# Kernel tuning notes

Hardware: AMD Instinct MI355X
Metric: run time of the kernel (lower is better)

The kernel has to match this reference:

```python
import jax, jax.numpy as jnp
import numpy as np

B, T, D, H, E, K = 4, 1024, 1024, 2048, 8, 2  # batch, tokens, model_dim, ffn hidden, experts, top-k


def setup_inputs() -> dict:
    key = jax.random.key(0)
    k0, k1, k2, k3 = jax.random.split(key, 4)
    return {
        "x": jax.random.normal(k0, (B, T, D), dtype=jnp.float32),
        "wg": jax.random.normal(k1, (D, E), dtype=jnp.float32) * 0.02,   # gate projection
        "w1": jax.random.normal(k2, (E, D, H), dtype=jnp.float32) * 0.02,  # expert fc1
        "b1": jnp.zeros((E, H), dtype=jnp.float32),
        "w2": jax.random.normal(k3, (E, H, D), dtype=jnp.float32) * 0.02,  # expert fc2
        "b2": jnp.zeros((E, D), dtype=jnp.float32),
    }


def _moe(x, wg, w1, b1, w2, b2):
    N = B * T
    xt = x.reshape(N, D)
    # --- gating: softmax scores, top-2 selection, normalize selected gates ---
    logits = xt @ wg                         # [N, E]
    scores = jax.nn.softmax(logits, axis=-1)
    vals, idx = jax.lax.top_k(scores, K)     # [N, K]
    vals = vals / jnp.sum(vals, axis=-1, keepdims=True)
    # combine weights: [N, E], nonzero only at the top-k experts per token
    combine = jnp.zeros((N, E), dtype=xt.dtype).at[
        jnp.arange(N)[:, None], idx
    ].add(vals)
    # --- expert FFN (activation_fn is identity per source) ---
    h = jnp.einsum('nd,edh->neh', xt, w1) + b1   # [N, E, H]
    o = jnp.einsum('neh,ehd->ned', h, w2) + b2   # [N, E, D]
    # --- combine / scatter back ---
    y = jnp.einsum('ne,ned->nd', combine, o)     # [N, D]
    return y.reshape(B, T, D)


def reference(x, wg, w1, b1, w2, b2):
    y = _moe(x, wg, w1, b1, w2, b2)              # [B, T, D]
    s = jnp.sum(y, axis=2)                       # [B, T]
    return jax.nn.log_softmax(s, axis=1)
```

## Files before the change

### kernel.cpp

```cpp
#include <hip/hip_runtime.h>
#include <stdint.h>

#define B_ 4
#define T_ 1024
#define D_ 1024
#define H_ 2048
#define E_ 8

__device__ __forceinline__ void stage16(const float* g, float* l) {
    __builtin_amdgcn_global_load_lds(
        (const __attribute__((address_space(1))) uint32_t*)g,
        (__attribute__((address_space(3))) uint32_t*)l, 16, 0, 0);
}

__global__ __launch_bounds__(256) void w2sum_kernel(const float* __restrict__ w2,
                                                    float* __restrict__ w2sum) {
    __shared__ float buf[3][4 * D_];
    const int wid = threadIdx.x >> 6, lane = threadIdx.x & 63;
    const float* src = w2 + ((size_t)blockIdx.x * 32 + wid) * D_ + lane * 4;

#define A_STAGE(k)                                                        \
    {                                                                     \
        const float* s_ = src + (size_t)(k) * 4 * D_;                     \
        float* d_ = &buf[(k) % 3][wid * D_];                              \
        stage16(s_,       d_);       stage16(s_ + 256, d_ + 256);         \
        stage16(s_ + 512, d_ + 512); stage16(s_ + 768, d_ + 768);         \
    }

    A_STAGE(0); A_STAGE(1);
    float accs[8];
#pragma unroll
    for (int k = 0; k < 8; ++k) {
        if (k < 7) asm volatile("s_waitcnt vmcnt(4)" ::: "memory");
        else       asm volatile("s_waitcnt vmcnt(0)" ::: "memory");
        if (k < 6) A_STAGE(k + 2);
        const float* row = &buf[k % 3][wid * D_];
        float acc = 0.f;
#pragma unroll
        for (int j = 0; j < 4; ++j) {
            float4 a = *(const float4*)&row[j * 256 + lane * 4];
            acc += a.x + a.y + a.z + a.w;
        }
#pragma unroll
        for (int off = 32; off >= 1; off >>= 1) acc += __shfl_xor(acc, off, 64);
        accs[k] = acc;
    }
#undef A_STAGE
    if (lane == 0) {
        const int r0 = blockIdx.x * 32 + wid;
#pragma unroll
        for (int k = 0; k < 8; ++k) w2sum[r0 + k * 4] = accs[k];
    }
}

__global__ __launch_bounds__(256) void v_build_kernel(const float* __restrict__ w1,
                                                      const float* __restrict__ w2sum,
                                                      const float* __restrict__ b1,
                                                      const float* __restrict__ b2,
                                                      float* __restrict__ vT,
                                                      float* __restrict__ c) {
    __shared__ float buf[2][4 * H_];
    const int bid = blockIdx.x;
    const int e   = bid >> 6;
    const int d0  = (bid & 63) * 16;
    const int wid = threadIdx.x >> 6, lane = threadIdx.x & 63;
    const float* src = w1 + ((size_t)e * D_ + d0 + wid) * H_ + lane * 4;

    const float4* wsp = (const float4*)(w2sum + (size_t)e * H_) + lane;
    float4 s0 = wsp[0],   s1 = wsp[64],  s2 = wsp[128], s3 = wsp[192],
           s4 = wsp[256], s5 = wsp[320], s6 = wsp[384], s7 = wsp[448];
    asm volatile("" ::: "memory");

#define B_STAGE(k)                                                         \
    {                                                                      \
        const float* s_ = src + (size_t)(k) * 4 * H_;                      \
        float* d_ = &buf[(k) & 1][wid * H_];                               \
        stage16(s_,        d_);        stage16(s_ + 256,  d_ + 256);       \
        stage16(s_ + 512,  d_ + 512);  stage16(s_ + 768,  d_ + 768);       \
        stage16(s_ + 1024, d_ + 1024); stage16(s_ + 1280, d_ + 1280);      \
        stage16(s_ + 1536, d_ + 1536); stage16(s_ + 1792, d_ + 1792);      \
    }

    B_STAGE(0); B_STAGE(1);
    float accs[4];
#pragma unroll
    for (int k = 0; k < 4; ++k) {
        if (k < 3) asm volatile("s_waitcnt vmcnt(8)" ::: "memory");
        else       asm volatile("s_waitcnt vmcnt(0)" ::: "memory");
        const float* row = &buf[k & 1][wid * H_];
        float acc;
        {
            float4 a0 = *(const float4*)&row[0 * 256 + lane * 4];
            float4 a1 = *(const float4*)&row[1 * 256 + lane * 4];
            float4 a2 = *(const float4*)&row[2 * 256 + lane * 4];
            float4 a3 = *(const float4*)&row[3 * 256 + lane * 4];
            float4 a4 = *(const float4*)&row[4 * 256 + lane * 4];
            float4 a5 = *(const float4*)&row[5 * 256 + lane * 4];
            float4 a6 = *(const float4*)&row[6 * 256 + lane * 4];
            float4 a7 = *(const float4*)&row[7 * 256 + lane * 4];
            acc = a0.x*s0.x + a0.y*s0.y + a0.z*s0.z + a0.w*s0.w
                + a1.x*s1.x + a1.y*s1.y + a1.z*s1.z + a1.w*s1.w
                + a2.x*s2.x + a2.y*s2.y + a2.z*s2.z + a2.w*s2.w
                + a3.x*s3.x + a3.y*s3.y + a3.z*s3.z + a3.w*s3.w
                + a4.x*s4.x + a4.y*s4.y + a4.z*s4.z + a4.w*s4.w
                + a5.x*s5.x + a5.y*s5.y + a5.z*s5.z + a5.w*s5.w
                + a6.x*s6.x + a6.y*s6.y + a6.z*s6.z + a6.w*s6.w
                + a7.x*s7.x + a7.y*s7.y + a7.z*s7.z + a7.w*s7.w;
        }
#pragma unroll
        for (int off = 32; off >= 1; off >>= 1) acc += __shfl_xor(acc, off, 64);
        accs[k] = acc;
        if (k < 2) B_STAGE(k + 2);
    }
#undef B_STAGE
    if (lane == 0) {
#pragma unroll
        for (int k = 0; k < 4; ++k)
            vT[(size_t)(d0 + k * 4 + wid) * E_ + e] = accs[k];
    }

    if ((bid & 63) == 0 && wid == 0) {
        const float4* bp = (const float4*)(b1 + (size_t)e * H_) + lane;
        float4 q0 = bp[0],   q1 = bp[64],  q2 = bp[128], q3 = bp[192],
               q4 = bp[256], q5 = bp[320], q6 = bp[384], q7 = bp[448];
        float s = q0.x*s0.x + q0.y*s0.y + q0.z*s0.z + q0.w*s0.w
                + q1.x*s1.x + q1.y*s1.y + q1.z*s1.z + q1.w*s1.w
                + q2.x*s2.x + q2.y*s2.y + q2.z*s2.z + q2.w*s2.w
                + q3.x*s3.x + q3.y*s3.y + q3.z*s3.z + q3.w*s3.w
                + q4.x*s4.x + q4.y*s4.y + q4.z*s4.z + q4.w*s4.w
                + q5.x*s5.x + q5.y*s5.y + q5.z*s5.z + q5.w*s5.w
                + q6.x*s6.x + q6.y*s6.y + q6.z*s6.z + q6.w*s6.w
                + q7.x*s7.x + q7.y*s7.y + q7.z*s7.z + q7.w*s7.w;
        const float4* cp = (const float4*)(b2 + (size_t)e * D_) + lane;
#pragma unroll
        for (int j = 0; j < 4; ++j) {
            float4 bb = cp[j * 64];
            s += bb.x + bb.y + bb.z + bb.w;
        }
#pragma unroll
        for (int off = 32; off >= 1; off >>= 1) s += __shfl_xor(s, off, 64);
        if (lane == 0) c[e] = s;
    }
}

__global__ __launch_bounds__(256) void token_kernel(
    const float* __restrict__ x,  const float* __restrict__ wg,
    const float* __restrict__ vT, const float* __restrict__ cbuf,
    float* __restrict__ sbuf)
{
    __shared__ float wgl[D_ * E_];
    __shared__ float vtl[D_ * E_];
    const int wid = threadIdx.x >> 6, lane = threadIdx.x & 63;

#pragma unroll
    for (int r = 0; r < 8; ++r) {
        int base = r * 1024 + wid * 256;
        stage16(wg + base + lane * 4, wgl + base);
        stage16(vT + base + lane * 4, vtl + base);
    }
    asm volatile("s_waitcnt vmcnt(0)" ::: "memory");
    __syncthreads();

    const int half = lane & 1;
    const int rrow = lane >> 1;

#pragma unroll
    for (int t = 0; t < 4; ++t) {
        const int n = blockIdx.x * 16 + wid * 4 + t;
        const float* xg = x + (size_t)n * D_ + rrow;
        float ag0 = 0.f, ag1 = 0.f, ag2 = 0.f, ag3 = 0.f;
        float av0 = 0.f, av1 = 0.f, av2 = 0.f, av3 = 0.f;
#pragma unroll
        for (int k = 0; k < 32; ++k) {
            float xs = xg[32 * k];
            const int o = (32 * k + rrow) * 8 + half * 4;
            float4 w4 = *(const float4*)&wgl[o];
            float4 v4 = *(const float4*)&vtl[o];
            ag0 += xs * w4.x; ag1 += xs * w4.y; ag2 += xs * w4.z; ag3 += xs * w4.w;
            av0 += xs * v4.x; av1 += xs * v4.y; av2 += xs * v4.z; av3 += xs * v4.w;
        }
#pragma unroll
        for (int off = 2; off <= 32; off <<= 1) {
            ag0 += __shfl_xor(ag0, off, 64); ag1 += __shfl_xor(ag1, off, 64);
            ag2 += __shfl_xor(ag2, off, 64); ag3 += __shfl_xor(ag3, off, 64);
            av0 += __shfl_xor(av0, off, 64); av1 += __shfl_xor(av1, off, 64);
            av2 += __shfl_xor(av2, off, 64); av3 += __shfl_xor(av3, off, 64);
        }
        float g4 = __shfl(ag0, 1, 64), g5 = __shfl(ag1, 1, 64),
              g6 = __shfl(ag2, 1, 64), g7 = __shfl(ag3, 1, 64);
        float h4 = __shfl(av0, 1, 64), h5 = __shfl(av1, 1, 64),
              h6 = __shfl(av2, 1, 64), h7 = __shfl(av3, 1, 64);
        if (lane == 0) {
            float lg[E_] = {ag0, ag1, ag2, ag3, g4, g5, g6, g7};
            float dv[E_] = {av0, av1, av2, av3, h4, h5, h6, h7};
            float m0 = lg[0]; int i0 = 0;
#pragma unroll
            for (int q = 1; q < E_; ++q) if (lg[q] > m0) { m0 = lg[q]; i0 = q; }
            float m1 = -3.0e38f; int i1 = 0;
#pragma unroll
            for (int q = 0; q < E_; ++q) if (q != i0 && lg[q] > m1) { m1 = lg[q]; i1 = q; }
            float dv0 = 0.f, dv1 = 0.f, c0v = 0.f, c1v = 0.f;
#pragma unroll
            for (int q = 0; q < E_; ++q) {
                if (q == i0) { dv0 += dv[q]; c0v += cbuf[q]; }
                if (q == i1) { dv1 += dv[q]; c1v += cbuf[q]; }
            }
            float g1w = 1.f / (1.f + expf(m0 - m1));
            sbuf[n] = (1.f - g1w) * (dv0 + c0v) + g1w * (dv1 + c1v);
        }
    }
}

__global__ __launch_bounds__(256) void lsm_kernel(const float* __restrict__ s,
                                                  float* __restrict__ out) {
    int brow = threadIdx.x >> 6;
    int lane = threadIdx.x & 63;
    const float* row = s + (size_t)brow * T_;
    float vals[16];
    float mx = -3.0e38f;
#pragma unroll
    for (int k = 0; k < 16; ++k) {
        vals[k] = row[lane + 64 * k];
        mx = fmaxf(mx, vals[k]);
    }
#pragma unroll
    for (int off = 32; off >= 1; off >>= 1) mx = fmaxf(mx, __shfl_xor(mx, off, 64));
    float sm = 0.f;
#pragma unroll
    for (int k = 0; k < 16; ++k) sm += expf(vals[k] - mx);
#pragma unroll
    for (int off = 32; off >= 1; off >>= 1) sm += __shfl_xor(sm, off, 64);
    float lse = mx + logf(sm);
#pragma unroll
    for (int k = 0; k < 16; ++k) out[(size_t)brow * T_ + lane + 64 * k] = vals[k] - lse;
}

extern "C" void kernel_launch(void* const* d_in, const int* in_sizes, int n_in,
                              void* d_out, int out_size, void* d_ws, size_t ws_size,
                              hipStream_t stream) {
    const float* x  = (const float*)d_in[0];
    const float* wg = (const float*)d_in[1];
    const float* w1 = (const float*)d_in[2];
    const float* b1 = (const float*)d_in[3];
    const float* w2 = (const float*)d_in[4];
    const float* b2 = (const float*)d_in[5];
    float* out = (float*)d_out;

    float* ws     = (float*)d_ws;
    float* w2sum  = ws;
    float* vT     = ws + 16384;
    float* cbuf   = ws + 24576;
    float* sbuf   = ws + 24592;

    w2sum_kernel<<<dim3(512), dim3(256), 0, stream>>>(w2, w2sum);
    v_build_kernel<<<dim3(512), dim3(256), 0, stream>>>(w1, w2sum, b1, b2, vT, cbuf);
    token_kernel<<<dim3(256), dim3(256), 0, stream>>>(x, wg, vT, cbuf, sbuf);
    lsm_kernel<<<dim3(1), dim3(256), 0, stream>>>(sbuf, out);
}
```

Baseline: 41.61 us.

## Fuse w2 row-sum and w1 projection into one kernel with atomic accumulation

Merges the w2 row-sum and the w1·w2sum projection into a single kernel. Each block owns a 32-wide slice of H for one expert, reduces the matching w2 rows into shared memory, then streams the w1 columns for that slice and accumulates partial vT and bias terms with atomicAdd. This drops one kernel launch and the global round trip of w2sum, at the cost of a memset and roughly a million atomic adds whose float ordering is nondeterministic. The token kernel also changes to process two tokens per wave over twice as many blocks, reusing the shared-memory weight loads across both tokens.

```diff
diff --git a/kernel.cpp b/kernel.cpp
--- a/kernel.cpp
+++ b/kernel.cpp
@@ -13,133 +13,104 @@
         (__attribute__((address_space(3))) uint32_t*)l, 16, 0, 0);
 }
 
-__global__ __launch_bounds__(256) void w2sum_kernel(const float* __restrict__ w2,
-                                                    float* __restrict__ w2sum) {
-    __shared__ float buf[3][4 * D_];
-    const int wid = threadIdx.x >> 6, lane = threadIdx.x & 63;
-    const float* src = w2 + ((size_t)blockIdx.x * 32 + wid) * D_ + lane * 4;
-
-#define A_STAGE(k)                                                        \
-    {                                                                     \
-        const float* s_ = src + (size_t)(k) * 4 * D_;                     \
-        float* d_ = &buf[(k) % 3][wid * D_];                              \
-        stage16(s_,       d_);       stage16(s_ + 256, d_ + 256);         \
-        stage16(s_ + 512, d_ + 512); stage16(s_ + 768, d_ + 768);         \
-    }
-
-    A_STAGE(0); A_STAGE(1);
-    float accs[8];
-#pragma unroll
-    for (int k = 0; k < 8; ++k) {
-        if (k < 7) asm volatile("s_waitcnt vmcnt(4)" ::: "memory");
-        else       asm volatile("s_waitcnt vmcnt(0)" ::: "memory");
-        if (k < 6) A_STAGE(k + 2);
-        const float* row = &buf[k % 3][wid * D_];
-        float acc = 0.f;
-#pragma unroll
-        for (int j = 0; j < 4; ++j) {
-            float4 a = *(const float4*)&row[j * 256 + lane * 4];
-            acc += a.x + a.y + a.z + a.w;
-        }
-#pragma unroll
-        for (int off = 32; off >= 1; off >>= 1) acc += __shfl_xor(acc, off, 64);
-        accs[k] = acc;
-    }
-#undef A_STAGE
-    if (lane == 0) {
-        const int r0 = blockIdx.x * 32 + wid;
-#pragma unroll
-        for (int k = 0; k < 8; ++k) w2sum[r0 + k * 4] = accs[k];
-    }
-}
-
-__global__ __launch_bounds__(256) void v_build_kernel(const float* __restrict__ w1,
-                                                      const float* __restrict__ w2sum,
-                                                      const float* __restrict__ b1,
-                                                      const float* __restrict__ b2,
-                                                      float* __restrict__ vT,
-                                                      float* __restrict__ c) {
-    __shared__ float buf[2][4 * H_];
+__global__ __launch_bounds__(256) void ab_kernel(
+    const float* __restrict__ w1, const float* __restrict__ b1,
+    const float* __restrict__ w2, const float* __restrict__ b2,
+    float* __restrict__ vT, float* __restrict__ cbuf)
+{
+    __shared__ float buf[3][4096];
+    __shared__ float wssum[32];
     const int bid = blockIdx.x;
     const int e   = bid >> 6;
-    const int d0  = (bid & 63) * 16;
+    const int j0  = (bid & 63) * 32;
     const int wid = threadIdx.x >> 6, lane = threadIdx.x & 63;
-    const float* src = w1 + ((size_t)e * D_ + d0 + wid) * H_ + lane * 4;
-
-    const float4* wsp = (const float4*)(w2sum + (size_t)e * H_) + lane;
-    float4 s0 = wsp[0],   s1 = wsp[64],  s2 = wsp[128], s3 = wsp[192],
-           s4 = wsp[256], s5 = wsp[320], s6 = wsp[384], s7 = wsp[448];
-    asm volatile("" ::: "memory");
-
-#define B_STAGE(k)                                                         \
-    {                                                                      \
-        const float* s_ = src + (size_t)(k) * 4 * H_;                      \
-        float* d_ = &buf[(k) & 1][wid * H_];                               \
-        stage16(s_,        d_);        stage16(s_ + 256,  d_ + 256);       \
-        stage16(s_ + 512,  d_ + 512);  stage16(s_ + 768,  d_ + 768);       \
-        stage16(s_ + 1024, d_ + 1024); stage16(s_ + 1280, d_ + 1280);      \
-        stage16(s_ + 1536, d_ + 1536); stage16(s_ + 1792, d_ + 1792);      \
-    }
-
-    B_STAGE(0); B_STAGE(1);
-    float accs[4];
-#pragma unroll
-    for (int k = 0; k < 4; ++k) {
-        if (k < 3) asm volatile("s_waitcnt vmcnt(8)" ::: "memory");
+
+    {
+        const float* src = w2 + ((size_t)(e * H_ + j0) + wid) * D_ + lane * 4;
+#define P1_STAGE(k) { const float* s_ = src + (size_t)(k) * 4 * D_;           \
+                      float* d_ = &buf[(k) % 3][wid * 1024];                  \
+                      stage16(s_, d_);         stage16(s_ + 256, d_ + 256);   \
+                      stage16(s_ + 512, d_ + 512); stage16(s_ + 768, d_ + 768); }
+        P1_STAGE(0); P1_STAGE(1);
+        float accs[8];
+#pragma unroll
+        for (int k = 0; k < 8; ++k) {
+            if (k < 7) asm volatile("s_waitcnt vmcnt(4)" ::: "memory");
+            else       asm volatile("s_waitcnt vmcnt(0)" ::: "memory");
+            if (k < 6) P1_STAGE(k + 2);
+            const float* row = &buf[k % 3][wid * 1024];
+            float acc = 0.f;
+#pragma unroll
+            for (int j = 0; j < 4; ++j) {
+                float4 a = *(const float4*)&row[j * 256 + lane * 4];
+                acc += a.x + a.y + a.z + a.w;
+            }
+#pragma unroll
+            for (int off = 32; off >= 1; off >>= 1) acc += __shfl_xor(acc, off, 64);
+            accs[k] = acc;
+        }
+#undef P1_STAGE
+        if (lane == 0) {
+#pragma unroll
+            for (int k = 0; k < 8; ++k) wssum[wid + k * 4] = accs[k];
+        }
+    }
+    __syncthreads();
+
+    const float4 wsv = *(const float4*)&wssum[(lane & 7) * 4];
+    const float* w1base = w1 + (size_t)e * D_ * H_ + j0 + (lane & 7) * 4;
+
+#define P2_STAGE(t) {                                                          \
+        const int rb_ = wid * 256 + (t) * 32;                                  \
+        float* d_ = &buf[(t) % 3][wid * 1024];                                 \
+        const float* s_ = w1base + (size_t)(rb_ + (lane >> 3)) * H_;           \
+        stage16(s_,               d_);                                         \
+        stage16(s_ + (size_t) 8 * H_, d_ + 256);                               \
+        stage16(s_ + (size_t)16 * H_, d_ + 512);                               \
+        stage16(s_ + (size_t)24 * H_, d_ + 768); }
+
+    P2_STAGE(0); P2_STAGE(1);
+    float p[8][4];
+#pragma unroll
+    for (int t = 0; t < 8; ++t) {
+        if (t < 7) asm volatile("s_waitcnt vmcnt(4)" ::: "memory");
         else       asm volatile("s_waitcnt vmcnt(0)" ::: "memory");
-        const float* row = &buf[k & 1][wid * H_];
-        float acc;
-        {
-            float4 a0 = *(const float4*)&row[0 * 256 + lane * 4];
-            float4 a1 = *(const float4*)&row[1 * 256 + lane * 4];
-            float4 a2 = *(const float4*)&row[2 * 256 + lane * 4];
-            float4 a3 = *(const float4*)&row[3 * 256 + lane * 4];
-            float4 a4 = *(const float4*)&row[4 * 256 + lane * 4];
-            float4 a5 = *(const float4*)&row[5 * 256 + lane * 4];
-            float4 a6 = *(const float4*)&row[6 * 256 + lane * 4];
-            float4 a7 = *(const float4*)&row[7 * 256 + lane * 4];
-            acc = a0.x*s0.x + a0.y*s0.y + a0.z*s0.z + a0.w*s0.w
-                + a1.x*s1.x + a1.y*s1.y + a1.z*s1.z + a1.w*s1.w
-                + a2.x*s2.x + a2.y*s2.y + a2.z*s2.z + a2.w*s2.w
-                + a3.x*s3.x + a3.y*s3.y + a3.z*s3.z + a3.w*s3.w
-                + a4.x*s4.x + a4.y*s4.y + a4.z*s4.z + a4.w*s4.w
-                + a5.x*s5.x + a5.y*s5.y + a5.z*s5.z + a5.w*s5.w
-                + a6.x*s6.x + a6.y*s6.y + a6.z*s6.z + a6.w*s6.w
-                + a7.x*s7.x + a7.y*s7.y + a7.z*s7.z + a7.w*s7.w;
-        }
-#pragma unroll
-        for (int off = 32; off >= 1; off >>= 1) acc += __shfl_xor(acc, off, 64);
-        accs[k] = acc;
-        if (k < 2) B_STAGE(k + 2);
-    }
-#undef B_STAGE
-    if (lane == 0) {
-#pragma unroll
-        for (int k = 0; k < 4; ++k)
-            vT[(size_t)(d0 + k * 4 + wid) * E_ + e] = accs[k];
-    }
-
-    if ((bid & 63) == 0 && wid == 0) {
-        const float4* bp = (const float4*)(b1 + (size_t)e * H_) + lane;
-        float4 q0 = bp[0],   q1 = bp[64],  q2 = bp[128], q3 = bp[192],
-               q4 = bp[256], q5 = bp[320], q6 = bp[384], q7 = bp[448];
-        float s = q0.x*s0.x + q0.y*s0.y + q0.z*s0.z + q0.w*s0.w
-                + q1.x*s1.x + q1.y*s1.y + q1.z*s1.z + q1.w*s1.w
-                + q2.x*s2.x + q2.y*s2.y + q2.z*s2.z + q2.w*s2.w
-                + q3.x*s3.x + q3.y*s3.y + q3.z*s3.z + q3.w*s3.w
-                + q4.x*s4.x + q4.y*s4.y + q4.z*s4.z + q4.w*s4.w
-                + q5.x*s5.x + q5.y*s5.y + q5.z*s5.z + q5.w*s5.w
-                + q6.x*s6.x + q6.y*s6.y + q6.z*s6.z + q6.w*s6.w
-                + q7.x*s7.x + q7.y*s7.y + q7.z*s7.z + q7.w*s7.w;
-        const float4* cp = (const float4*)(b2 + (size_t)e * D_) + lane;
-#pragma unroll
-        for (int j = 0; j < 4; ++j) {
-            float4 bb = cp[j * 64];
-            s += bb.x + bb.y + bb.z + bb.w;
-        }
-#pragma unroll
-        for (int off = 32; off >= 1; off >>= 1) s += __shfl_xor(s, off, 64);
-        if (lane == 0) c[e] = s;
+        if (t < 6) P2_STAGE(t + 2);
+        const float* dat = &buf[t % 3][wid * 1024];
+#pragma unroll
+        for (int s = 0; s < 4; ++s) {
+            float4 a = *(const float4*)&dat[s * 256 + lane * 4];
+            float v = a.x * wsv.x + a.y * wsv.y + a.z * wsv.z + a.w * wsv.w;
+            v += __shfl_xor(v, 1, 64);
+            v += __shfl_xor(v, 2, 64);
+            v += __shfl_xor(v, 4, 64);
+            p[t][s] = v;
+        }
+    }
+#undef P2_STAGE
+
+    if ((lane & 7) == 0) {
+        const int m = lane >> 3;
+#pragma unroll
+        for (int t = 0; t < 8; ++t)
+#pragma unroll
+            for (int s = 0; s < 4; ++s)
+                atomicAdd(&vT[(size_t)(wid * 256 + t * 32 + s * 8 + m) * E_ + e],
+                          p[t][s]);
+    }
+
+    if (wid == 0) {
+        float tt = (lane < 32) ? b1[(size_t)e * H_ + j0 + lane] * wssum[lane] : 0.f;
+#pragma unroll
+        for (int off = 32; off >= 1; off >>= 1) tt += __shfl_xor(tt, off, 64);
+        if (lane == 0) atomicAdd(&cbuf[e], tt);
+    }
+    if ((bid & 63) == 0 && wid == 1) {
+        float tt = 0.f;
+        for (int k = lane; k < D_; k += 64) tt += b2[(size_t)e * D_ + k];
+#pragma unroll
+        for (int off = 32; off >= 1; off >>= 1) tt += __shfl_xor(tt, off, 64);
+        if (lane == 0) atomicAdd(&cbuf[e], tt);
     }
 }
 
@@ -164,35 +135,60 @@
     const int half = lane & 1;
     const int rrow = lane >> 1;
 
-#pragma unroll
-    for (int t = 0; t < 4; ++t) {
-        const int n = blockIdx.x * 16 + wid * 4 + t;
-        const float* xg = x + (size_t)n * D_ + rrow;
-        float ag0 = 0.f, ag1 = 0.f, ag2 = 0.f, ag3 = 0.f;
-        float av0 = 0.f, av1 = 0.f, av2 = 0.f, av3 = 0.f;
-#pragma unroll
-        for (int k = 0; k < 32; ++k) {
-            float xs = xg[32 * k];
-            const int o = (32 * k + rrow) * 8 + half * 4;
-            float4 w4 = *(const float4*)&wgl[o];
-            float4 v4 = *(const float4*)&vtl[o];
-            ag0 += xs * w4.x; ag1 += xs * w4.y; ag2 += xs * w4.z; ag3 += xs * w4.w;
-            av0 += xs * v4.x; av1 += xs * v4.y; av2 += xs * v4.z; av3 += xs * v4.w;
-        }
-#pragma unroll
-        for (int off = 2; off <= 32; off <<= 1) {
-            ag0 += __shfl_xor(ag0, off, 64); ag1 += __shfl_xor(ag1, off, 64);
-            ag2 += __shfl_xor(ag2, off, 64); ag3 += __shfl_xor(ag3, off, 64);
-            av0 += __shfl_xor(av0, off, 64); av1 += __shfl_xor(av1, off, 64);
-            av2 += __shfl_xor(av2, off, 64); av3 += __shfl_xor(av3, off, 64);
-        }
-        float g4 = __shfl(ag0, 1, 64), g5 = __shfl(ag1, 1, 64),
-              g6 = __shfl(ag2, 1, 64), g7 = __shfl(ag3, 1, 64);
-        float h4 = __shfl(av0, 1, 64), h5 = __shfl(av1, 1, 64),
-              h6 = __shfl(av2, 1, 64), h7 = __shfl(av3, 1, 64);
-        if (lane == 0) {
-            float lg[E_] = {ag0, ag1, ag2, ag3, g4, g5, g6, g7};
-            float dv[E_] = {av0, av1, av2, av3, h4, h5, h6, h7};
+    const int nA = blockIdx.x * 8 + wid * 2;
+    const float* xga = x + (size_t)nA * D_ + rrow;
+    const float* xgb = xga + D_;
+
+    float agA[4] = {0,0,0,0}, avA[4] = {0,0,0,0};
+    float agB[4] = {0,0,0,0}, avB[4] = {0,0,0,0};
+
+#pragma unroll
+    for (int k = 0; k < 32; ++k) {
+        float xa = xga[32 * k];
+        float xb = xgb[32 * k];
+        const int o = (32 * k + rrow) * 8 + half * 4;
+        float4 w4 = *(const float4*)&wgl[o];
+        float4 v4 = *(const float4*)&vtl[o];
+        agA[0] += xa * w4.x; agA[1] += xa * w4.y; agA[2] += xa * w4.z; agA[3] += xa * w4.w;
+        avA[0] += xa * v4.x; avA[1] += xa * v4.y; avA[2] += xa * v4.z; avA[3] += xa * v4.w;
+        agB[0] += xb * w4.x; agB[1] += xb * w4.y; agB[2] += xb * w4.z; agB[3] += xb * w4.w;
+        avB[0] += xb * v4.x; avB[1] += xb * v4.y; avB[2] += xb * v4.z; avB[3] += xb * v4.w;
+    }
+
+#pragma unroll
+    for (int off = 2; off <= 32; off <<= 1) {
+#pragma unroll
+        for (int q = 0; q < 4; ++q) {
+            agA[q] += __shfl_xor(agA[q], off, 64);
+            avA[q] += __shfl_xor(avA[q], off, 64);
+            agB[q] += __shfl_xor(agB[q], off, 64);
+            avB[q] += __shfl_xor(avB[q], off, 64);
+        }
+    }
+    float gA4 = __shfl(agA[0], 1, 64), gA5 = __shfl(agA[1], 1, 64),
+          gA6 = __shfl(agA[2], 1, 64), gA7 = __shfl(agA[3], 1, 64);
+    float hA4 = __shfl(avA[0], 1, 64), hA5 = __shfl(avA[1], 1, 64),
+          hA6 = __shfl(avA[2], 1, 64), hA7 = __shfl(avA[3], 1, 64);
+    float gB4 = __shfl(agB[0], 1, 64), gB5 = __shfl(agB[1], 1, 64),
+          gB6 = __shfl(agB[2], 1, 64), gB7 = __shfl(agB[3], 1, 64);
+    float hB4 = __shfl(avB[0], 1, 64), hB5 = __shfl(avB[1], 1, 64),
+          hB6 = __shfl(avB[2], 1, 64), hB7 = __shfl(avB[3], 1, 64);
+
+    if (lane == 0) {
+#pragma unroll
+        for (int tok = 0; tok < 2; ++tok) {
+            float lg[E_], dv[E_];
+            if (tok == 0) {
+                lg[0]=agA[0]; lg[1]=agA[1]; lg[2]=agA[2]; lg[3]=agA[3];
+                lg[4]=gA4;    lg[5]=gA5;    lg[6]=gA6;    lg[7]=gA7;
+                dv[0]=avA[0]; dv[1]=avA[1]; dv[2]=avA[2]; dv[3]=avA[3];
+                dv[4]=hA4;    dv[5]=hA5;    dv[6]=hA6;    dv[7]=hA7;
+            } else {
+                lg[0]=agB[0]; lg[1]=agB[1]; lg[2]=agB[2]; lg[3]=agB[3];
+                lg[4]=gB4;    lg[5]=gB5;    lg[6]=gB6;    lg[7]=gB7;
+                dv[0]=avB[0]; dv[1]=avB[1]; dv[2]=avB[2]; dv[3]=avB[3];
+                dv[4]=hB4;    dv[5]=hB5;    dv[6]=hB6;    dv[7]=hB7;
+            }
             float m0 = lg[0]; int i0 = 0;
 #pragma unroll
             for (int q = 1; q < E_; ++q) if (lg[q] > m0) { m0 = lg[q]; i0 = q; }
@@ -206,7 +202,7 @@
                 if (q == i1) { dv1 += dv[q]; c1v += cbuf[q]; }
             }
             float g1w = 1.f / (1.f + expf(m0 - m1));
-            sbuf[n] = (1.f - g1w) * (dv0 + c0v) + g1w * (dv1 + c1v);
+            sbuf[nA + tok] = (1.f - g1w) * (dv0 + c0v) + g1w * (dv1 + c1v);
         }
     }
 }
@@ -246,14 +242,14 @@
     const float* b2 = (const float*)d_in[5];
     float* out = (float*)d_out;
 
-    float* ws     = (float*)d_ws;
-    float* w2sum  = ws;
-    float* vT     = ws + 16384;
-    float* cbuf   = ws + 24576;
-    float* sbuf   = ws + 24592;
-
-    w2sum_kernel<<<dim3(512), dim3(256), 0, stream>>>(w2, w2sum);
-    v_build_kernel<<<dim3(512), dim3(256), 0, stream>>>(w1, w2sum, b1, b2, vT, cbuf);
-    token_kernel<<<dim3(256), dim3(256), 0, stream>>>(x, wg, vT, cbuf, sbuf);
+    float* ws   = (float*)d_ws;
+    float* vT   = ws;
+    float* cbuf = ws + 8192;
+    float* sbuf = ws + 8200;
+
+    hipMemsetAsync(vT, 0, (8192 + 8) * sizeof(float), stream);
+
+    ab_kernel<<<dim3(512), dim3(256), 0, stream>>>(w1, b1, w2, b2, vT, cbuf);
+    token_kernel<<<dim3(512), dim3(256), 0, stream>>>(x, wg, vT, cbuf, sbuf);
     lsm_kernel<<<dim3(1), dim3(256), 0, stream>>>(sbuf, out);
 }
```

Result: slower. 53.44 us (+28.4%).
